# Optimization experiments

Measured on AMD Instinct MI355X. Metric: run time of the kernel, lower is better.

## Reference

```python
import jax, jax.numpy as jnp
import numpy as np

N_NODES = 100000
D_IN = 128
D_HID = 128
N_EDGES = 1600000


def setup_inputs() -> dict:
    key = jax.random.key(0)
    ks = jax.random.split(key, 8)
    x = jax.random.normal(ks[0], (N_NODES, D_IN), dtype=jnp.float32)
    edge_index = jax.random.randint(ks[1], (2, N_EDGES), 0, N_NODES, dtype=jnp.int64)
    s = 1.0 / np.sqrt(D_IN)
    W1l = jax.random.uniform(ks[2], (D_IN, D_HID), jnp.float32, -s, s)
    W1r = jax.random.uniform(ks[3], (D_IN, D_HID), jnp.float32, -s, s)
    b1 = jnp.zeros((D_HID,), jnp.float32)
    sh = 1.0 / np.sqrt(D_HID)
    W2l = jax.random.uniform(ks[4], (D_HID, D_HID), jnp.float32, -sh, sh)
    W2r = jax.random.uniform(ks[5], (D_HID, D_HID), jnp.float32, -sh, sh)
    b2 = jnp.zeros((D_HID,), jnp.float32)
    return {"x": x, "edge_index": edge_index, "W1l": W1l, "W1r": W1r,
            "b1": b1, "W2l": W2l, "W2r": W2r, "b2": b2}


def _sage_conv(x, src, dst, Wl, Wr, b, n_nodes):
    # mean-aggregate neighbor features: gather x[src], scatter-add at dst
    msgs = x[src]                                                  # [E, D]
    agg = jax.ops.segment_sum(msgs, dst, num_segments=n_nodes)    # [N, D]
    cnt = jax.ops.segment_sum(jnp.ones((src.shape[0],), x.dtype), dst,
                              num_segments=n_nodes)               # [N]
    agg = agg / jnp.maximum(cnt, 1.0)[:, None]
    # SAGEConv: lin_l(aggregated) + lin_r(root) + bias
    return agg @ Wl + x @ Wr + b


def reference(x, edge_index, W1l, W1r, b1, W2l, W2r, b2):
    src, dst = edge_index[0], edge_index[1]
    n = x.shape[0]
    h = jax.nn.relu(_sage_conv(x, src, dst, W1l, W1r, b1, n))
    return _sage_conv(h, src, dst, W2l, W2r, b2, n)
```

## Files before the change

### kernel.cpp

```cpp
#include <hip/hip_runtime.h>

#define D 128
constexpr int TILE_ROWS  = 64;
constexpr int BUCKET_CAP = 2048;
constexpr int LDS_STRIDE = 136;

constexpr int SB_SHIFT   = 11;
constexpr int SB_MASK    = (1 << SB_SHIFT) - 1;
constexpr int MAX_NSB    = 52;
constexpr int SB_CAP     = 40960;
constexpr int CNT_STRIDE = 32;
constexpr int P1_CHUNK   = 4096;
constexpr int P1_CAP     = 192;
constexpr int P2_CHUNK   = 4096;
constexpr int P2_KBLK    = 12;
constexpr int P2_CAP     = 192;

using bf16x8 = __attribute__((ext_vector_type(8))) short;
using f32x4  = __attribute__((ext_vector_type(4))) float;
typedef float f32x2_t __attribute__((ext_vector_type(2)));

static __device__ __forceinline__ unsigned short f2bf(float f) {
    unsigned int u = __float_as_uint(f);
    unsigned int r = (u + 0x7FFFu + ((u >> 16) & 1u)) >> 16;
    return (unsigned short)r;
}

__global__ __launch_bounds__(256)
void bin_pass1(const int* __restrict__ src, const int* __restrict__ dst,
               int* __restrict__ gcnt, int* __restrict__ sbent, int E, int nsb) {
    __shared__ int fifo[MAX_NSB][P1_CAP];
    __shared__ int fcnt[MAX_NSB];

    const int tid  = threadIdx.x;
    const int base = blockIdx.x * P1_CHUNK;

    for (int i = tid; i < nsb; i += 256) fcnt[i] = 0;
    __syncthreads();

    int ds[16], ss[16];
    #pragma unroll
    for (int q = 0; q < 16; ++q) {
        const int e = base + q * 256 + tid;
        const bool v = e < E;
        ds[q] = v ? dst[e] : -1;
        ss[q] = v ? src[e] : 0;
    }
    #pragma unroll
    for (int q = 0; q < 16; ++q) {
        if (ds[q] < 0) continue;
        const int sb = ds[q] >> SB_SHIFT;
        const int entry = (ss[q] << SB_SHIFT) | (ds[q] & SB_MASK);
        const int pos = atomicAdd(&fcnt[sb], 1);
        if (pos < P1_CAP) {
            fifo[sb][pos] = entry;
        } else {
            const int gp = atomicAdd(&gcnt[sb * CNT_STRIDE], 1);
            if (gp < SB_CAP) sbent[(size_t)sb * SB_CAP + gp] = entry;
        }
    }
    __syncthreads();

    const int wid = tid >> 6, lane = tid & 63;
    for (int sb = wid; sb < nsb; sb += 4) {
        int n = fcnt[sb];
        if (n > P1_CAP) n = P1_CAP;
        if (n == 0) continue;
        int gbase;
        if (lane == 0) gbase = atomicAdd(&gcnt[sb * CNT_STRIDE], n);
        gbase = __shfl(gbase, 0, 64);
        for (int i = lane; i < n; i += 64)
            if (gbase + i < SB_CAP)
                sbent[(size_t)sb * SB_CAP + gbase + i] = fifo[sb][i];
    }
}

__global__ __launch_bounds__(256)
void bin_pass2(const int* __restrict__ gcnt, const int* __restrict__ sbent,
               int* __restrict__ tcnt, int* __restrict__ buckets) {
    __shared__ int fifo[32][P2_CAP];
    __shared__ int fcnt[32];

    const int sb = blockIdx.x / P2_KBLK;
    const int c  = blockIdx.x % P2_KBLK;
    const int n  = min(gcnt[sb * CNT_STRIDE], SB_CAP);
    const int beg = c * P2_CHUNK;
    const int end = min(beg + P2_CHUNK, n);
    if (beg >= end) return;

    const int tid = threadIdx.x;
    if (tid < 32) fcnt[tid] = 0;
    __syncthreads();

    for (int i = beg + tid; i < end; i += 256) {
        const int entry = sbent[(size_t)sb * SB_CAP + i];
        const int dl = entry & SB_MASK;
        const int t  = dl >> 6;
        const int out = ((entry >> SB_SHIFT) << 6) | (dl & 63);
        const int pos = atomicAdd(&fcnt[t], 1);
        if (pos < P2_CAP) {
            fifo[t][pos] = out;
        } else {
            const int tile = sb * 32 + t;
            const int gp = atomicAdd(&tcnt[tile], 1);
            if (gp < BUCKET_CAP) buckets[(size_t)tile * BUCKET_CAP + gp] = out;
        }
    }
    __syncthreads();

    const int wid = tid >> 6, lane = tid & 63;
    for (int t = wid; t < 32; t += 4) {
        int n2 = fcnt[t];
        if (n2 > P2_CAP) n2 = P2_CAP;
        if (n2 == 0) continue;
        const int tile = sb * 32 + t;
        int gbase;
        if (lane == 0) gbase = atomicAdd(&tcnt[tile], n2);
        gbase = __shfl(gbase, 0, 64);
        for (int i = lane; i < n2; i += 64)
            if (gbase + i < BUCKET_CAP)
                buckets[(size_t)tile * BUCKET_CAP + gbase + i] = fifo[t][i];
    }
}

__global__ void cast_x(const float* __restrict__ x, unsigned short* __restrict__ xb,
                       unsigned int* __restrict__ xf8, int n4) {
    int i = blockIdx.x * blockDim.x + threadIdx.x;
    if (i >= n4) return;
    const float4 v = *(const float4*)(x + (size_t)i * 4);
    ushort4 o;
    o.x = f2bf(v.x); o.y = f2bf(v.y); o.z = f2bf(v.z); o.w = f2bf(v.w);
    *(ushort4*)(xb + (size_t)i * 4) = o;
    int p = __builtin_amdgcn_cvt_pk_fp8_f32(v.x, v.y, 0, false);
    p     = __builtin_amdgcn_cvt_pk_fp8_f32(v.z, v.w, p, true);
    xf8[i] = (unsigned int)p;
}

__global__ void wswz_kernel(const float* __restrict__ W1l, const float* __restrict__ W1r,
                            const float* __restrict__ W2l, const float* __restrict__ W2r,
                            unsigned short* __restrict__ Wsw) {
    int idx = blockIdx.x * blockDim.x + threadIdx.x;
    if (idx >= 2 * 8 * 8 * 64 * 8) return;
    const int j  = idx & 7;
    const int l  = (idx >> 3) & 63;
    const int t  = (idx >> 9) & 7;
    const int kc = (idx >> 12) & 7;
    const int L  = idx >> 15;
    const int k  = (kc & 3) * 32 + 8 * (l >> 4) + j;
    const int n  = t * 16 + (l & 15);
    const float* W = L ? ((kc < 4) ? W2l : W2r) : ((kc < 4) ? W1l : W1r);
    Wsw[idx] = f2bf(W[k * D + n]);
}

template <bool RELU, bool BF16OUT, bool F8OUT>
__global__ __launch_bounds__(256)
void sage_layer(const unsigned short* __restrict__ Xb,
                const unsigned int* __restrict__ Xf8,
                const int* __restrict__ tcnt,
                const int* __restrict__ buckets,
                const unsigned short* __restrict__ Wsw,
                const float* __restrict__ bias,
                void* __restrict__ outv,
                unsigned char* __restrict__ outf8,
                int N) {
    __shared__ unsigned short sAgg[TILE_ROWS * LDS_STRIDE];
    __shared__ int lists[BUCKET_CAP];
    __shared__ int cnt64[TILE_ROWS], off64[TILE_ROWS], cur64[TILE_ROWS];

    const int tid = threadIdx.x;
    const int b   = blockIdx.x;
    const int rowBase = b * TILE_ROWS;

    const int nE = min(tcnt[b], BUCKET_CAP);
    if (tid < 64) { cnt64[tid] = 0; cur64[tid] = 0; }
    __syncthreads();
    const int* myb = buckets + (size_t)b * BUCKET_CAP;
    for (int i = tid; i < nE; i += 256) atomicAdd(&cnt64[myb[i] & 63], 1);
    __syncthreads();
    if (tid < 64) {
        const int v = cnt64[tid];
        int incl = v;
        #pragma unroll
        for (int o = 1; o < 64; o <<= 1) {
            const int t = __shfl_up(incl, o, 64);
            if (tid >= o) incl += t;
        }
        off64[tid] = incl - v;
    }
    __syncthreads();
    for (int i = tid; i < nE; i += 256) {
        const int p = myb[i];
        const int d = p & 63;
        const int pos = off64[d] + atomicAdd(&cur64[d], 1);
        lists[pos] = p >> 6;
    }
    __syncthreads();

    const int wid  = tid >> 6;
    const int lane = tid & 63;
    const int half = lane >> 5;
    const int c4   = lane & 31;

    for (int t = 0; t < 16; ++t) {
        const int ld   = wid * 16 + t;
        const int deg  = cnt64[ld];
        const int base = off64[ld];
        float a0 = 0.f, a1 = 0.f, a2 = 0.f, a3 = 0.f;
        for (int i = 0; i < deg; i += 16) {
            unsigned int u[8];
            #pragma unroll
            for (int q = 0; q < 8; ++q) {
                const int e = i + 2 * q + half;
                const bool valid = e < deg;
                const int s = lists[valid ? (base + e) : 0];
                const unsigned int val = Xf8[(size_t)s * 32 + c4];
                u[q] = valid ? val : 0u;
            }
            #pragma unroll
            for (int q = 0; q < 8; ++q) {
                const f32x2_t lo = __builtin_amdgcn_cvt_pk_f32_fp8((int)u[q], false);
                const f32x2_t hi = __builtin_amdgcn_cvt_pk_f32_fp8((int)u[q], true);
                a0 += lo[0]; a1 += lo[1]; a2 += hi[0]; a3 += hi[1];
            }
        }
        a0 += __shfl_xor(a0, 32, 64);
        a1 += __shfl_xor(a1, 32, 64);
        a2 += __shfl_xor(a2, 32, 64);
        a3 += __shfl_xor(a3, 32, 64);
        const float rd = (deg > 0) ? 1.0f / (float)deg : 0.f;
        if (lane < 32) {
            const unsigned int w0 = (unsigned int)f2bf(a0 * rd) |
                                    ((unsigned int)f2bf(a1 * rd) << 16);
            const unsigned int w1 = (unsigned int)f2bf(a2 * rd) |
                                    ((unsigned int)f2bf(a3 * rd) << 16);
            unsigned int* p = (unsigned int*)&sAgg[ld * LDS_STRIDE + c4 * 4];
            p[0] = w0; p[1] = w1;
        }
    }
    __syncthreads();

    const int r16  = lane & 15;
    const int koff = (lane >> 4) * 8;
    int arow = rowBase + wid * 16 + r16;
    if (arow >= N) arow = N - 1;
    const unsigned short* Wp = Wsw + lane * 8;

    f32x4 acc[8] = {};
    #pragma unroll
    for (int kc = 0; kc < 8; ++kc) {
        const int k0 = (kc & 3) * 32;
        bf16x8 afrag;
        if (kc < 4)
            afrag = *(const bf16x8*)(&sAgg[(wid * 16 + r16) * LDS_STRIDE + k0 + koff]);
        else
            afrag = *(const bf16x8*)(Xb + (size_t)arow * D + k0 + koff);
        #pragma unroll
        for (int t = 0; t < 8; ++t) {
            const bf16x8 bfrag = *(const bf16x8*)(Wp + (size_t)(kc * 8 + t) * 512);
            acc[t] = __builtin_amdgcn_mfma_f32_16x16x32_bf16(afrag, bfrag, acc[t], 0, 0, 0);
        }
    }

    const int mBase = rowBase + wid * 16 + 4 * (lane >> 4);
    const int nSub  = lane & 15;
    #pragma unroll
    for (int t = 0; t < 8; ++t) {
        const int n = t * 16 + nSub;
        const float bv = bias[n];
        #pragma unroll
        for (int r = 0; r < 4; ++r) {
            const int m = mBase + r;
            if (m < N) {
                float v = acc[t][r] + bv;
                if (RELU) v = fmaxf(v, 0.f);
                if (BF16OUT)
                    ((unsigned short*)outv)[(size_t)m * D + n] = f2bf(v);
                else
                    ((float*)outv)[(size_t)m * D + n] = v;
                if (F8OUT) {
                    const int pk = __builtin_amdgcn_cvt_pk_fp8_f32(v, 0.f, 0, false);
                    outf8[(size_t)m * D + n] = (unsigned char)(pk & 0xFF);
                }
            }
        }
    }
}

extern "C" void kernel_launch(void* const* d_in, const int* in_sizes, int n_in,
                              void* d_out, int out_size, void* d_ws, size_t ws_size,
                              hipStream_t stream) {
    const float* x   = (const float*)d_in[0];
    const int*  edge = (const int*)d_in[1];
    const float* W1l = (const float*)d_in[2];
    const float* W1r = (const float*)d_in[3];
    const float* b1  = (const float*)d_in[4];
    const float* W2l = (const float*)d_in[5];
    const float* W2r = (const float*)d_in[6];
    const float* b2  = (const float*)d_in[7];
    float* out = (float*)d_out;

    const int N = in_sizes[0] / D;
    const int E = in_sizes[1] / 2;
    const int* src = edge;
    const int* dst = edge + E;
    const int nbuckets = (N + TILE_ROWS - 1) / TILE_ROWS;
    const int nsb = (N + (1 << SB_SHIFT) - 1) >> SB_SHIFT;

    char* ws = (char*)d_ws;
    auto alignup = [](size_t v) { return (v + 255) & ~(size_t)255; };
    int* gcnt    = (int*)ws;             ws += alignup((size_t)MAX_NSB * CNT_STRIDE * 4);
    int* tcnt    = (int*)ws;             ws += alignup((size_t)nbuckets * 4);
    int* sbent   = (int*)ws;             ws += alignup((size_t)MAX_NSB * SB_CAP * 4);
    int* buckets = (int*)ws;             ws += alignup((size_t)nbuckets * BUCKET_CAP * 4);
    unsigned short* xb  = (unsigned short*)ws;  ws += alignup((size_t)N * D * 2);
    unsigned int*   xf8 = (unsigned int*)ws;    ws += alignup((size_t)N * D);
    unsigned short* hb  = (unsigned short*)ws;  ws += alignup((size_t)N * D * 2);
    unsigned char*  hf8 = (unsigned char*)ws;   ws += alignup((size_t)N * D);
    unsigned short* Wsw = (unsigned short*)ws;  ws += alignup((size_t)65536 * 2);

    hipMemsetAsync(gcnt, 0, (size_t)MAX_NSB * CNT_STRIDE * 4, stream);
    hipMemsetAsync(tcnt, 0, (size_t)nbuckets * 4, stream);

    const int n4 = N * D / 4;
    cast_x<<<(n4 + 255) / 256, 256, 0, stream>>>(x, xb, xf8, n4);
    wswz_kernel<<<65536 / 256, 256, 0, stream>>>(W1l, W1r, W2l, W2r, Wsw);

    bin_pass1<<<(E + P1_CHUNK - 1) / P1_CHUNK, 256, 0, stream>>>(src, dst, gcnt, sbent, E, nsb);
    bin_pass2<<<nsb * P2_KBLK, 256, 0, stream>>>(gcnt, sbent, tcnt, buckets);

    sage_layer<true, true, true><<<nbuckets, 256, 0, stream>>>(
        xb, xf8, tcnt, buckets, Wsw, b1, hb, hf8, N);
    sage_layer<false, false, false><<<nbuckets, 256, 0, stream>>>(
        hb, (const unsigned int*)hf8, tcnt, buckets, Wsw + 32768, b2, out, nullptr, N);
}
```

Baseline: 220.5 us.

## Batch gathers across four destination rows and preload bucket entries into registers

```diff
diff --git a/kernel.cpp b/kernel.cpp
--- a/kernel.cpp
+++ b/kernel.cpp
@@ -172,10 +172,18 @@
     const int rowBase = b * TILE_ROWS;
 
     const int nE = min(tcnt[b], BUCKET_CAP);
+    const int* myb = buckets + (size_t)b * BUCKET_CAP;
+    int ent[8];
+    #pragma unroll
+    for (int q = 0; q < 8; ++q) {
+        const int i = tid + q * 256;
+        ent[q] = (i < nE) ? myb[i] : -1;
+    }
     if (tid < 64) { cnt64[tid] = 0; cur64[tid] = 0; }
     __syncthreads();
-    const int* myb = buckets + (size_t)b * BUCKET_CAP;
-    for (int i = tid; i < nE; i += 256) atomicAdd(&cnt64[myb[i] & 63], 1);
+    #pragma unroll
+    for (int q = 0; q < 8; ++q)
+        if (ent[q] >= 0) atomicAdd(&cnt64[ent[q] & 63], 1);
     __syncthreads();
     if (tid < 64) {
         const int v = cnt64[tid];
@@ -188,12 +196,12 @@
         off64[tid] = incl - v;
     }
     __syncthreads();
-    for (int i = tid; i < nE; i += 256) {
-        const int p = myb[i];
-        const int d = p & 63;
-        const int pos = off64[d] + atomicAdd(&cur64[d], 1);
-        lists[pos] = p >> 6;
-    }
+    #pragma unroll
+    for (int q = 0; q < 8; ++q)
+        if (ent[q] >= 0) {
+            const int d = ent[q] & 63;
+            lists[off64[d] + atomicAdd(&cur64[d], 1)] = ent[q] >> 6;
+        }
     __syncthreads();
 
     const int wid  = tid >> 6;
@@ -201,40 +209,60 @@
     const int half = lane >> 5;
     const int c4   = lane & 31;
 
-    for (int t = 0; t < 16; ++t) {
-        const int ld   = wid * 16 + t;
-        const int deg  = cnt64[ld];
-        const int base = off64[ld];
-        float a0 = 0.f, a1 = 0.f, a2 = 0.f, a3 = 0.f;
-        for (int i = 0; i < deg; i += 16) {
-            unsigned int u[8];
+    for (int g = 0; g < 4; ++g) {
+        int dg[4], bs[4];
+        int nbmax = 0;
+        #pragma unroll
+        for (int n = 0; n < 4; ++n) {
+            const int ld = wid * 16 + g * 4 + n;
+            dg[n] = cnt64[ld];
+            bs[n] = off64[ld];
+            nbmax = max(nbmax, (dg[n] + 15) >> 4);
+        }
+        f32x2_t s01[4], s23[4];
+        #pragma unroll
+        for (int n = 0; n < 4; ++n) { s01[n] = 0.f; s23[n] = 0.f; }
+
+        for (int bb = 0; bb < nbmax; ++bb) {
+            unsigned int u[4][8];
             #pragma unroll
-            for (int q = 0; q < 8; ++q) {
-                const int e = i + 2 * q + half;
-                const bool valid = e < deg;
-                const int s = lists[valid ? (base + e) : 0];
-                const unsigned int val = Xf8[(size_t)s * 32 + c4];
-                u[q] = valid ? val : 0u;
+            for (int n = 0; n < 4; ++n) {
+                #pragma unroll
+                for (int q = 0; q < 8; ++q) {
+                    const int e = bb * 16 + 2 * q + half;
+                    unsigned int v = 0;
+                    if (e < dg[n])
+                        v = Xf8[(size_t)lists[bs[n] + e] * 32 + c4];
+                    u[n][q] = v;
+                }
             }
             #pragma unroll
-            for (int q = 0; q < 8; ++q) {
-                const f32x2_t lo = __builtin_amdgcn_cvt_pk_f32_fp8((int)u[q], false);
-                const f32x2_t hi = __builtin_amdgcn_cvt_pk_f32_fp8((int)u[q], true);
-                a0 += lo[0]; a1 += lo[1]; a2 += hi[0]; a3 += hi[1];
+            for (int n = 0; n < 4; ++n) {
+                #pragma unroll
+                for (int q = 0; q < 8; ++q) {
+                    s01[n] += __builtin_amdgcn_cvt_pk_f32_fp8((int)u[n][q], false);
+                    s23[n] += __builtin_amdgcn_cvt_pk_f32_fp8((int)u[n][q], true);
+                }
             }
         }
-        a0 += __shfl_xor(a0, 32, 64);
-        a1 += __shfl_xor(a1, 32, 64);
-        a2 += __shfl_xor(a2, 32, 64);
-        a3 += __shfl_xor(a3, 32, 64);
-        const float rd = (deg > 0) ? 1.0f / (float)deg : 0.f;
-        if (lane < 32) {
-            const unsigned int w0 = (unsigned int)f2bf(a0 * rd) |
-                                    ((unsigned int)f2bf(a1 * rd) << 16);
-            const unsigned int w1 = (unsigned int)f2bf(a2 * rd) |
-                                    ((unsigned int)f2bf(a3 * rd) << 16);
-            unsigned int* p = (unsigned int*)&sAgg[ld * LDS_STRIDE + c4 * 4];
-            p[0] = w0; p[1] = w1;
+
+        #pragma unroll
+        for (int n = 0; n < 4; ++n) {
+            float a0 = s01[n][0], a1 = s01[n][1], a2 = s23[n][0], a3 = s23[n][1];
+            a0 += __shfl_xor(a0, 32, 64);
+            a1 += __shfl_xor(a1, 32, 64);
+            a2 += __shfl_xor(a2, 32, 64);
+            a3 += __shfl_xor(a3, 32, 64);
+            const int deg = dg[n];
+            const float rd = (deg > 0) ? 1.0f / (float)deg : 0.f;
+            if (lane < 32) {
+                const unsigned int w0 = (unsigned int)f2bf(a0 * rd) |
+                                        ((unsigned int)f2bf(a1 * rd) << 16);
+                const unsigned int w1 = (unsigned int)f2bf(a2 * rd) |
+                                        ((unsigned int)f2bf(a3 * rd) << 16);
+                unsigned int* p = (unsigned int*)&sAgg[(wid * 16 + g * 4 + n) * LDS_STRIDE + c4 * 4];
+                p[0] = w0; p[1] = w1;
+            }
         }
     }
     __syncthreads();
```

Result: faster. 208.1 us (-5.7%).
